# Kernel optimization log

Measured on AMD Instinct MI355X. Metric: run time of the kernel, lower is better.

## Reference

```python
import jax, jax.numpy as jnp
import numpy as np

B, S, D = 4, 4096, 1024

def setup_inputs() -> dict:
    key = jax.random.key(0)
    ks = jax.random.split(key, 5)
    scale = 1.0 / np.sqrt(D)
    return {
        "query": jax.random.normal(ks[0], (B, S, D), dtype=jnp.float32),
        "key": jax.random.normal(ks[1], (B, S, D), dtype=jnp.float32),
        "value": jax.random.normal(ks[2], (B, S, D), dtype=jnp.float32),
        "W": jax.random.normal(ks[3], (D, D), dtype=jnp.float32) * scale,  # torch Linear weight [out,in]
        "b": jax.random.normal(ks[4], (D,), dtype=jnp.float32) * 0.01,
    }

def reference(query, key, value, W, b):
    # shared projection (same_embd=True): q = Q W^T + b, same W,b for k,v
    q = jnp.einsum('bsd,od->bso', query, W) + b
    k = jnp.einsum('bsd,od->bso', key, W) + b
    v = jnp.einsum('bsd,od->bso', value, W) + b
    # unscaled dot-product attention (scaled=False default)
    a = jnp.einsum('bto,bso->bts', q, k)  # [B, tgt, src]
    attn = jax.nn.softmax(a, axis=2)
    output = jnp.einsum('bts,bso->bto', attn, v)
    return (output, attn)
```

## Files before the change

### kernel.cpp

```cpp
#include <hip/hip_runtime.h>
#include <hip/hip_bf16.h>
#include <hip/hip_fp16.h>

#define BD 4
#define SS 4096
#define DD 1024
#define RTOT (BD*SS)

typedef _Float16 f16;
typedef __attribute__((ext_vector_type(8))) _Float16 f16x8;
typedef __attribute__((ext_vector_type(4))) float f32x4;

static __device__ __forceinline__ unsigned short f2h(float f) {
  f16 h = (f16)f;
  return __builtin_bit_cast(unsigned short, h);
}
static __device__ __forceinline__ float h2f(unsigned short u) {
  return (float)__builtin_bit_cast(f16, u);
}

static __device__ __forceinline__ void gload16(const void* g, void* l) {
  __builtin_amdgcn_global_load_lds(
      (const __attribute__((address_space(1))) unsigned int*)g,
      (__attribute__((address_space(3))) unsigned int*)l, 16, 0, 0);
}

__global__ __launch_bounds__(256)
void convx_kernel(const float* __restrict__ q, const float* __restrict__ k,
                  const float* __restrict__ v,
                  unsigned short* __restrict__ xq, unsigned short* __restrict__ xk,
                  unsigned short* __restrict__ xv) {
  const float* src = blockIdx.z == 0 ? q : (blockIdx.z == 1 ? k : v);
  unsigned short* dst = blockIdx.z == 0 ? xq : (blockIdx.z == 1 ? xk : xv);
  const int n4 = RTOT * DD / 4;
  for (int i = blockIdx.x * 256 + threadIdx.x; i < n4; i += gridDim.x * 256) {
    float4 x = reinterpret_cast<const float4*>(src)[i];
    ushort4 h;
    h.x = f2h(x.x); h.y = f2h(x.y); h.z = f2h(x.z); h.w = f2h(x.w);
    reinterpret_cast<ushort4*>(dst)[i] = h;
  }
}

__global__ void split_w_kernel(const float* __restrict__ W,
                               unsigned short* __restrict__ Wh,
                               unsigned short* __restrict__ Wl) {
  int i = (blockIdx.x * 256 + threadIdx.x) * 4;
  float4 x = *reinterpret_cast<const float4*>(W + i);
  ushort4 h, l;
  h.x = f2h(x.x); l.x = f2h(x.x - h2f(h.x));
  h.y = f2h(x.y); l.y = f2h(x.y - h2f(h.y));
  h.z = f2h(x.z); l.z = f2h(x.z - h2f(h.z));
  h.w = f2h(x.w); l.w = f2h(x.w - h2f(h.w));
  *reinterpret_cast<ushort4*>(Wh + i) = h;
  *reinterpret_cast<ushort4*>(Wl + i) = l;
}

template<int TERMS, int EPI>
__global__ __launch_bounds__(512, 2)
void proj_one(const unsigned short* __restrict__ Xf,
              const unsigned short* __restrict__ Wh,
              const unsigned short* __restrict__ Wl,
              const float* __restrict__ bias,
              unsigned short* __restrict__ O1, unsigned short* __restrict__ O2)
{
  constexpr int OPS = 1 + TERMS;
  __shared__ unsigned short lds[2 * OPS][8192];
  const int tid = threadIdx.x, lane = tid & 63, wid = tid >> 6;
  const int t0 = blockIdx.x * 256;
  const int n0 = blockIdx.y * 256;

  const int sfr = (tid >> 2) & 15;
  const int scc = (tid & 3) ^ ((sfr >> 1) & 3);
  const int srowl = (tid >> 6) * 16 + sfr;
  const size_t aoff = (size_t)(t0 + srowl) * DD + scc * 8;
  const size_t boff = (size_t)(n0 + srowl) * DD + scc * 8;
  const int l0s = tid * 8;
  const int l1s = 4096 + tid * 8;

#define PSTAGE(cur, k0)  do { \
    gload16(Xf + aoff + (k0),          &lds[(cur)*OPS+0][l0s]); \
    gload16(Xf + aoff + 131072 + (k0), &lds[(cur)*OPS+0][l1s]); \
    gload16(Wh + boff + (k0),          &lds[(cur)*OPS+1][l0s]); \
    gload16(Wh + boff + 131072 + (k0), &lds[(cur)*OPS+1][l1s]); \
    if (TERMS == 2) { \
      gload16(Wl + boff + (k0),          &lds[(cur)*OPS+2][l0s]); \
      gload16(Wl + boff + 131072 + (k0), &lds[(cur)*OPS+2][l1s]); \
    } \
  } while (0)

  const int wr = wid >> 2, wc = wid & 3;
  const int rfr = lane & 15, rcc = lane >> 4;
  const int lp8 = (rfr * 4 + (rcc ^ ((rfr >> 1) & 3))) * 8;

  f32x4 acc[8][4] = {};

  int cur = 0;
  PSTAGE(0, 0);
  __syncthreads();

  for (int t = 0; t < 32; ++t) {
    if (t < 31) PSTAGE(cur ^ 1, (t + 1) * 32);

    f16x8 bhf[4], blf[4];
#pragma unroll
    for (int n = 0; n < 4; ++n) {
      bhf[n] = *reinterpret_cast<const f16x8*>(&lds[cur * OPS + 1][(wc * 4 + n) * 512 + lp8]);
      if (TERMS == 2)
        blf[n] = *reinterpret_cast<const f16x8*>(&lds[cur * OPS + 2][(wc * 4 + n) * 512 + lp8]);
    }
#pragma unroll
    for (int h = 0; h < 2; ++h) {
      f16x8 ahf[4];
#pragma unroll
      for (int m = 0; m < 4; ++m)
        ahf[m] = *reinterpret_cast<const f16x8*>(&lds[cur * OPS + 0][(wr * 8 + h * 4 + m) * 512 + lp8]);
      __builtin_amdgcn_s_setprio(1);
#pragma unroll
      for (int m = 0; m < 4; ++m)
#pragma unroll
        for (int n = 0; n < 4; ++n) {
          acc[h * 4 + m][n] = __builtin_amdgcn_mfma_f32_16x16x32_f16(ahf[m], bhf[n], acc[h * 4 + m][n], 0, 0, 0);
          if (TERMS == 2)
            acc[h * 4 + m][n] = __builtin_amdgcn_mfma_f32_16x16x32_f16(ahf[m], blf[n], acc[h * 4 + m][n], 0, 0, 0);
        }
      __builtin_amdgcn_s_setprio(0);
    }
    __syncthreads();
    cur ^= 1;
  }
#undef PSTAGE

  const int col = lane & 15, rb = (lane >> 4) * 4;
#pragma unroll
  for (int m = 0; m < 8; ++m)
#pragma unroll
    for (int n = 0; n < 4; ++n) {
      int oc = n0 + wc * 64 + n * 16 + col;
      float bv = bias[oc];
      if (EPI == 2) {
        int tr = t0 + wr * 128 + m * 16 + rb;
        int bb = tr >> 12, s = tr & (SS - 1);
        ushort4 h;
        h.x = f2h(acc[m][n][0] + bv);
        h.y = f2h(acc[m][n][1] + bv);
        h.z = f2h(acc[m][n][2] + bv);
        h.w = f2h(acc[m][n][3] + bv);
        *reinterpret_cast<ushort4*>(O1 + ((size_t)(bb * DD + oc)) * SS + s) = h;
      } else {
#pragma unroll
        for (int q = 0; q < 4; ++q) {
          int tr = t0 + wr * 128 + m * 16 + rb + q;
          float p = acc[m][n][q] + bv;
          if (EPI == 0) {
            O1[(size_t)tr * DD + oc] = f2h(p);
          } else {
            unsigned short h = f2h(p);
            O1[(size_t)tr * DD + oc] = h;
            O2[(size_t)tr * DD + oc] = f2h(p - h2f(h));
          }
        }
      }
    }
}

__global__ __launch_bounds__(512, 2)
void logits_v3(const unsigned short* __restrict__ qf,
               const unsigned short* __restrict__ kh, const unsigned short* __restrict__ kl,
               float* __restrict__ out)
{
  __shared__ unsigned short lds[6][8192];
  const int tid = threadIdx.x, lane = tid & 63, wid = tid >> 6;

  int bid = blockIdx.x;
  int swz = (bid & 7) * 128 + (bid >> 3);
  const int b = swz >> 8;
  const int r = swz & 255;
  const int t0 = (r >> 4) * 256, s0 = (r & 15) * 256;

  const unsigned short* qB  = qf + (size_t)b * SS * DD;
  const unsigned short* khB = kh + (size_t)b * SS * DD;
  const unsigned short* klB = kl + (size_t)b * SS * DD;

  const int sfr = (tid >> 2) & 15;
  const int scc = (tid & 3) ^ ((sfr >> 1) & 3);
  const int srowl = (tid >> 6) * 16 + sfr;
  const size_t qoff0 = (size_t)(t0 + srowl) * DD + scc * 8;
  const size_t koff0 = (size_t)(s0 + srowl) * DD + scc * 8;
  const int l0s = tid * 8;
  const int l1s = 4096 + tid * 8;

#define STAGE(cur, k0)  do { \
    gload16(qB  + qoff0 + (k0),          &lds[(cur)*3+0][l0s]); \
    gload16(qB  + qoff0 + 131072 + (k0), &lds[(cur)*3+0][l1s]); \
    gload16(khB + koff0 + (k0),          &lds[(cur)*3+1][l0s]); \
    gload16(khB + koff0 + 131072 + (k0), &lds[(cur)*3+1][l1s]); \
    gload16(klB + koff0 + (k0),          &lds[(cur)*3+2][l0s]); \
    gload16(klB + koff0 + 131072 + (k0), &lds[(cur)*3+2][l1s]); \
  } while (0)

  const int wr = wid >> 2, wc = wid & 3;
  const int rfr = lane & 15, rcc = lane >> 4;
  const int lp8 = (rfr * 4 + (rcc ^ ((rfr >> 1) & 3))) * 8;

  f32x4 acc[8][4] = {};

  int cur = 0;
  STAGE(0, 0);
  __syncthreads();

  for (int t = 0; t < 32; ++t) {
    if (t < 31) STAGE(cur ^ 1, (t + 1) * 32);

    f16x8 bhf[4], blf[4];
#pragma unroll
    for (int n = 0; n < 4; ++n) {
      bhf[n] = *reinterpret_cast<const f16x8*>(&lds[cur * 3 + 1][(wc * 4 + n) * 512 + lp8]);
      blf[n] = *reinterpret_cast<const f16x8*>(&lds[cur * 3 + 2][(wc * 4 + n) * 512 + lp8]);
    }
#pragma unroll
    for (int h = 0; h < 2; ++h) {
      f16x8 ahf[4];
#pragma unroll
      for (int m = 0; m < 4; ++m)
        ahf[m] = *reinterpret_cast<const f16x8*>(&lds[cur * 3 + 0][(wr * 8 + h * 4 + m) * 512 + lp8]);
      __builtin_amdgcn_s_setprio(1);
#pragma unroll
      for (int m = 0; m < 4; ++m)
#pragma unroll
        for (int n = 0; n < 4; ++n) {
          acc[h * 4 + m][n] = __builtin_amdgcn_mfma_f32_16x16x32_f16(ahf[m], bhf[n], acc[h * 4 + m][n], 0, 0, 0);
          acc[h * 4 + m][n] = __builtin_amdgcn_mfma_f32_16x16x32_f16(ahf[m], blf[n], acc[h * 4 + m][n], 0, 0, 0);
        }
      __builtin_amdgcn_s_setprio(0);
    }
    __syncthreads();
    cur ^= 1;
  }
#undef STAGE

  const int col = lane & 15, rb = (lane >> 4) * 4;
#pragma unroll
  for (int m = 0; m < 8; ++m)
#pragma unroll
    for (int n = 0; n < 4; ++n) {
      int s = s0 + wc * 64 + n * 16 + col;
#pragma unroll
      for (int q = 0; q < 4; ++q) {
        int tr = t0 + wr * 128 + m * 16 + rb + q;
        out[((size_t)b * SS + tr) * SS + s] = acc[m][n][q];
      }
    }
}

__global__ __launch_bounds__(256)
void softmax_kernel(float* __restrict__ attn) {
  float* rp = attn + (size_t)blockIdx.x * SS;
  const int tid = threadIdx.x, lane = tid & 63, wid = tid >> 6;
  float v[16];
  float m = -1e30f;
#pragma unroll
  for (int i = 0; i < 4; ++i) {
    float4 x = *reinterpret_cast<const float4*>(rp + i * 1024 + tid * 4);
    v[i * 4 + 0] = x.x; v[i * 4 + 1] = x.y; v[i * 4 + 2] = x.z; v[i * 4 + 3] = x.w;
    m = fmaxf(m, fmaxf(fmaxf(x.x, x.y), fmaxf(x.z, x.w)));
  }
#pragma unroll
  for (int off = 32; off; off >>= 1) m = fmaxf(m, __shfl_xor(m, off));
  __shared__ float redm[4], reds[4];
  if (lane == 0) redm[wid] = m;
  __syncthreads();
  m = fmaxf(fmaxf(redm[0], redm[1]), fmaxf(redm[2], redm[3]));
  float sum = 0.f;
#pragma unroll
  for (int i = 0; i < 16; ++i) { v[i] = __expf(v[i] - m); sum += v[i]; }
#pragma unroll
  for (int off = 32; off; off >>= 1) sum += __shfl_xor(sum, off);
  if (lane == 0) reds[wid] = sum;
  __syncthreads();
  float inv = 1.0f / (reds[0] + reds[1] + reds[2] + reds[3]);
#pragma unroll
  for (int i = 0; i < 4; ++i) {
    float4 x;
    x.x = v[i * 4 + 0] * inv; x.y = v[i * 4 + 1] * inv;
    x.z = v[i * 4 + 2] * inv; x.w = v[i * 4 + 3] * inv;
    *reinterpret_cast<float4*>(rp + i * 1024 + tid * 4) = x;
  }
}

__global__ __launch_bounds__(512)
void pv_v3(const float* __restrict__ attn, const unsigned short* __restrict__ vT,
           float* __restrict__ out)
{
  __shared__ unsigned short As[128][40];
  __shared__ unsigned short Bs[16384];
  const int tid = threadIdx.x, lane = tid & 63, wid = tid >> 6;

  int bx = blockIdx.x;
  bx = (bx & 7) * 4 + (bx >> 3);
  const int t0 = bx * 128;
  const int nH = blockIdx.y * 512;
  const int b = blockIdx.z;
  const float* aB = attn + ((size_t)b * SS + t0) * SS;
  const unsigned short* vB = vT + ((size_t)b * DD + nH) * SS;

  const int wr = wid >> 2, wc = wid & 3;

  const int sfr = (tid >> 2) & 15;
  const int scc = (tid & 3) ^ ((sfr >> 1) & 3);
  const int brow = (tid >> 6) * 16 + sfr;

  f32x4 acc[4][8] = {};

  for (int s0 = 0; s0 < SS; s0 += 32) {
    __syncthreads();
#pragma unroll
    for (int rnd = 0; rnd < 2; ++rnd) {
      int e = rnd * 512 + tid;
      int r = e >> 3, c = (e & 7) * 4;
      float4 x = *reinterpret_cast<const float4*>(aB + (size_t)r * SS + s0 + c);
      ushort4 h;
      h.x = f2h(x.x); h.y = f2h(x.y); h.z = f2h(x.z); h.w = f2h(x.w);
      *reinterpret_cast<ushort4*>(&As[r][c]) = h;
    }
#pragma unroll
    for (int g = 0; g < 4; ++g)
      gload16(vB + (size_t)(brow + g * 128) * SS + s0 + scc * 8,
              &Bs[0] + (size_t)g * 4096 + (size_t)tid * 8);
    __syncthreads();

    f16x8 a[4], bb[8];
    const int fr = lane & 15, kb = (lane >> 4) * 8;
    const int lp8 = (fr * 4 + ((lane >> 4) ^ ((fr >> 1) & 3))) * 8;
#pragma unroll
    for (int m = 0; m < 4; ++m)
      a[m] = *reinterpret_cast<const f16x8*>(&As[wr * 64 + m * 16 + fr][kb]);
#pragma unroll
    for (int n = 0; n < 8; ++n)
      bb[n] = *reinterpret_cast<const f16x8*>(&Bs[(wc * 8 + n) * 512 + lp8]);

    __builtin_amdgcn_s_setprio(1);
#pragma unroll
    for (int m = 0; m < 4; ++m)
#pragma unroll
      for (int n = 0; n < 8; ++n)
        acc[m][n] = __builtin_amdgcn_mfma_f32_16x16x32_f16(a[m], bb[n], acc[m][n], 0, 0, 0);
    __builtin_amdgcn_s_setprio(0);
  }

  const int col = lane & 15, rb = (lane >> 4) * 4;
#pragma unroll
  for (int m = 0; m < 4; ++m)
#pragma unroll
    for (int n = 0; n < 8; ++n) {
      int o = nH + wc * 128 + n * 16 + col;
#pragma unroll
      for (int q = 0; q < 4; ++q) {
        int t = t0 + wr * 64 + m * 16 + rb + q;
        out[((size_t)b * SS + t) * DD + o] = acc[m][n][q];
      }
    }
}

extern "C" void kernel_launch(void* const* d_in, const int* in_sizes, int n_in,
                              void* d_out, int out_size, void* d_ws, size_t ws_size,
                              hipStream_t stream) {
  const float* query = (const float*)d_in[0];
  const float* key   = (const float*)d_in[1];
  const float* value = (const float*)d_in[2];
  const float* W     = (const float*)d_in[3];
  const float* bias  = (const float*)d_in[4];

  float* out  = (float*)d_out;
  float* attn = out + (size_t)BD * SS * DD;

  unsigned short* Whf = (unsigned short*)d_ws;
  unsigned short* Wlf = Whf + (size_t)DD * DD;
  unsigned short* xq  = Wlf + (size_t)DD * DD;
  unsigned short* xk  = xq  + (size_t)RTOT * DD;
  unsigned short* xv  = xk  + (size_t)RTOT * DD;
  unsigned short* qfb = xv  + (size_t)RTOT * DD;
  unsigned short* khi = qfb + (size_t)RTOT * DD;
  unsigned short* klo = khi + (size_t)RTOT * DD;
  unsigned short* vT  = xq;

  convx_kernel<<<dim3(2048, 1, 3), 256, 0, stream>>>(query, key, value, xq, xk, xv);
  split_w_kernel<<<DD * DD / (256 * 4), 256, 0, stream>>>(W, Whf, Wlf);

  dim3 gp(RTOT / 256, DD / 256);
  proj_one<2, 0><<<gp, 512, 0, stream>>>(xq, Whf, Wlf, bias, qfb, nullptr);
  proj_one<2, 1><<<gp, 512, 0, stream>>>(xk, Whf, Wlf, bias, khi, klo);
  proj_one<1, 2><<<gp, 512, 0, stream>>>(xv, Whf, nullptr, bias, vT, nullptr);

  logits_v3<<<(SS / 256) * (SS / 256) * BD, 512, 0, stream>>>(qfb, khi, klo, attn);
  softmax_kernel<<<RTOT, 256, 0, stream>>>(attn);
  pv_v3<<<dim3(SS / 128, DD / 512, BD), 512, 0, stream>>>(attn, vT, out);
}
```

Baseline: 812.0 us.

## Double-buffer PV kernel and halve row tile to 64 for occupancy

The attention-times-V kernel now double-buffers its LDS tiles. The next V tile is loaded asynchronously and the next fp32 attention slice is prefetched into registers while MFMAs run on the current buffer, which drops one barrier per iteration. The row tile shrinks from 128 to 64, so each wave holds a 64x64 accumulator instead of 64x128. Launch bounds request two blocks per CU and the grid doubles in x. This aims to hide global-load latency and raise occupancy, at the cost of re-reading V twice as often across blocks.

```diff
diff --git a/kernel.cpp b/kernel.cpp
--- a/kernel.cpp
+++ b/kernel.cpp
@@ -287,75 +287,88 @@
   }
 }
 
-__global__ __launch_bounds__(512)
-void pv_v3(const float* __restrict__ attn, const unsigned short* __restrict__ vT,
+__global__ __launch_bounds__(512, 2)
+void pv_v4(const float* __restrict__ attn, const unsigned short* __restrict__ vT,
            float* __restrict__ out)
 {
-  __shared__ unsigned short As[128][40];
-  __shared__ unsigned short Bs[16384];
+  __shared__ unsigned short As[2][64][40];
+  __shared__ unsigned short Bs[2][16384];
   const int tid = threadIdx.x, lane = tid & 63, wid = tid >> 6;
 
-  int bx = blockIdx.x;
-  bx = (bx & 7) * 4 + (bx >> 3);
-  const int t0 = bx * 128;
+  int bid = blockIdx.x;
+  int bx = (bid & 7) * 8 + (bid >> 3);
+  const int t0 = bx * 64;
   const int nH = blockIdx.y * 512;
   const int b = blockIdx.z;
   const float* aB = attn + ((size_t)b * SS + t0) * SS;
   const unsigned short* vB = vT + ((size_t)b * DD + nH) * SS;
 
-  const int wr = wid >> 2, wc = wid & 3;
-
+  const int arow = tid >> 3, acol = (tid & 7) * 4;
   const int sfr = (tid >> 2) & 15;
   const int scc = (tid & 3) ^ ((sfr >> 1) & 3);
   const int brow = (tid >> 6) * 16 + sfr;
 
-  f32x4 acc[4][8] = {};
-
-  for (int s0 = 0; s0 < SS; s0 += 32) {
-    __syncthreads();
-#pragma unroll
-    for (int rnd = 0; rnd < 2; ++rnd) {
-      int e = rnd * 512 + tid;
-      int r = e >> 3, c = (e & 7) * 4;
-      float4 x = *reinterpret_cast<const float4*>(aB + (size_t)r * SS + s0 + c);
-      ushort4 h;
-      h.x = f2h(x.x); h.y = f2h(x.y); h.z = f2h(x.z); h.w = f2h(x.w);
-      *reinterpret_cast<ushort4*>(&As[r][c]) = h;
-    }
-#pragma unroll
-    for (int g = 0; g < 4; ++g)
-      gload16(vB + (size_t)(brow + g * 128) * SS + s0 + scc * 8,
-              &Bs[0] + (size_t)g * 4096 + (size_t)tid * 8);
-    __syncthreads();
-
-    f16x8 a[4], bb[8];
+  f32x4 acc[4][4] = {};
+  float4 areg;
+
+#define PVB_LOAD(buf, s0) do { \
+    _Pragma("unroll") \
+    for (int g = 0; g < 4; ++g) \
+      gload16(vB + (size_t)(brow + g * 128) * SS + (s0) + scc * 8, \
+              &Bs[buf][0] + (size_t)g * 4096 + (size_t)tid * 8); \
+  } while (0)
+#define PVA_WRITE(buf) do { \
+    ushort4 h; \
+    h.x = f2h(areg.x); h.y = f2h(areg.y); h.z = f2h(areg.z); h.w = f2h(areg.w); \
+    *reinterpret_cast<ushort4*>(&As[buf][arow][acol]) = h; \
+  } while (0)
+
+  PVB_LOAD(0, 0);
+  areg = *reinterpret_cast<const float4*>(aB + (size_t)arow * SS + acol);
+  PVA_WRITE(0);
+  __syncthreads();
+
+  int cur = 0;
+  for (int it = 0; it < 128; ++it) {
+    if (it < 127) {
+      PVB_LOAD(cur ^ 1, (it + 1) * 32);
+      areg = *reinterpret_cast<const float4*>(aB + (size_t)arow * SS + (it + 1) * 32 + acol);
+    }
+
+    f16x8 a[4], bb[4];
     const int fr = lane & 15, kb = (lane >> 4) * 8;
     const int lp8 = (fr * 4 + ((lane >> 4) ^ ((fr >> 1) & 3))) * 8;
 #pragma unroll
     for (int m = 0; m < 4; ++m)
-      a[m] = *reinterpret_cast<const f16x8*>(&As[wr * 64 + m * 16 + fr][kb]);
-#pragma unroll
-    for (int n = 0; n < 8; ++n)
-      bb[n] = *reinterpret_cast<const f16x8*>(&Bs[(wc * 8 + n) * 512 + lp8]);
+      a[m] = *reinterpret_cast<const f16x8*>(&As[cur][m * 16 + fr][kb]);
+#pragma unroll
+    for (int n = 0; n < 4; ++n)
+      bb[n] = *reinterpret_cast<const f16x8*>(&Bs[cur][(wid * 4 + n) * 512 + lp8]);
 
     __builtin_amdgcn_s_setprio(1);
 #pragma unroll
     for (int m = 0; m < 4; ++m)
 #pragma unroll
-      for (int n = 0; n < 8; ++n)
+      for (int n = 0; n < 4; ++n)
         acc[m][n] = __builtin_amdgcn_mfma_f32_16x16x32_f16(a[m], bb[n], acc[m][n], 0, 0, 0);
     __builtin_amdgcn_s_setprio(0);
-  }
+
+    if (it < 127) PVA_WRITE(cur ^ 1);
+    __syncthreads();
+    cur ^= 1;
+  }
+#undef PVB_LOAD
+#undef PVA_WRITE
 
   const int col = lane & 15, rb = (lane >> 4) * 4;
 #pragma unroll
   for (int m = 0; m < 4; ++m)
 #pragma unroll
-    for (int n = 0; n < 8; ++n) {
-      int o = nH + wc * 128 + n * 16 + col;
+    for (int n = 0; n < 4; ++n) {
+      int o = nH + wid * 64 + n * 16 + col;
 #pragma unroll
       for (int q = 0; q < 4; ++q) {
-        int t = t0 + wr * 64 + m * 16 + rb + q;
+        int t = t0 + m * 16 + rb + q;
         out[((size_t)b * SS + t) * DD + o] = acc[m][n][q];
       }
     }
@@ -393,5 +406,5 @@
 
   logits_v3<<<(SS / 256) * (SS / 256) * BD, 512, 0, stream>>>(qfb, khi, klo, attn);
   softmax_kernel<<<RTOT, 256, 0, stream>>>(attn);
-  pv_v3<<<dim3(SS / 128, DD / 512, BD), 512, 0, stream>>>(attn, vT, out);
-}
+  pv_v4<<<dim3(SS / 64, DD / 512, BD), 512, 0, stream>>>(attn, vT, out);
+}
```

Measured after the change: 811.4 us. No clear change (-0.1%).

## Double-buffer PV GEMM with register-prefetched attn and 256x256 tiles

Applied to the files above, without the earlier changes.

Rewrites the attention-times-V kernel to use 256x256 output tiles with a K step of 64, double-buffered LDS, and a register prefetch of the next fp32 attn tile. That tile is converted to fp16 and written to LDS after the MFMAs, which overlaps global loads with compute and halves the barriers per K. A new 1D block swizzle groups tiles across batch for cache locality. The cost is heavier register pressure (32 accumulators plus 8 float4 prefetch registers) and 128KB of LDS per block, which may limit occupancy.

```diff
diff --git a/kernel.cpp b/kernel.cpp
--- a/kernel.cpp
+++ b/kernel.cpp
@@ -288,74 +288,115 @@
 }
 
 __global__ __launch_bounds__(512)
-void pv_v3(const float* __restrict__ attn, const unsigned short* __restrict__ vT,
+void pv_v5(const float* __restrict__ attn, const unsigned short* __restrict__ vT,
            float* __restrict__ out)
 {
-  __shared__ unsigned short As[128][40];
-  __shared__ unsigned short Bs[16384];
+  __shared__ unsigned short lds[8][8192];
   const int tid = threadIdx.x, lane = tid & 63, wid = tid >> 6;
 
-  int bx = blockIdx.x;
-  bx = (bx & 7) * 4 + (bx >> 3);
-  const int t0 = bx * 128;
-  const int nH = blockIdx.y * 512;
-  const int b = blockIdx.z;
+  int bid = blockIdx.x;
+  int swz = (bid & 7) * 32 + (bid >> 3);
+  const int b = swz >> 6, rem = swz & 63;
+  const int t0 = (rem >> 2) * 256;
+  const int n0 = (rem & 3) * 256;
   const float* aB = attn + ((size_t)b * SS + t0) * SS;
-  const unsigned short* vB = vT + ((size_t)b * DD + nH) * SS;
-
-  const int wr = wid >> 2, wc = wid & 3;
+  const unsigned short* vB = vT + ((size_t)b * DD + n0) * SS;
 
   const int sfr = (tid >> 2) & 15;
   const int scc = (tid & 3) ^ ((sfr >> 1) & 3);
-  const int brow = (tid >> 6) * 16 + sfr;
-
-  f32x4 acc[4][8] = {};
-
-  for (int s0 = 0; s0 < SS; s0 += 32) {
+  const int srowl = (tid >> 6) * 16 + sfr;
+  const size_t row0 = (size_t)srowl * SS;
+  const size_t row1 = (size_t)(srowl + 128) * SS;
+  const int l0s = tid * 8, l1s = 4096 + tid * 8;
+
+  const int wr = wid >> 2, wc = wid & 3;
+  const int rfr = lane & 15, rcc = lane >> 4;
+  const int lp8 = (rfr * 4 + (rcc ^ ((rfr >> 1) & 3))) * 8;
+
+  f32x4 acc[8][4] = {};
+  float4 ar[8];
+
+#define PV5_BLOAD(buf, k0) do { \
+    gload16(vB + row0 + (k0) + scc * 8,      &lds[(buf)*4+2][l0s]); \
+    gload16(vB + row1 + (k0) + scc * 8,      &lds[(buf)*4+2][l1s]); \
+    gload16(vB + row0 + (k0) + 32 + scc * 8, &lds[(buf)*4+3][l0s]); \
+    gload16(vB + row1 + (k0) + 32 + scc * 8, &lds[(buf)*4+3][l1s]); \
+  } while (0)
+
+#define PV5_ALOAD(k0) do { \
+    ar[0] = *reinterpret_cast<const float4*>(aB + row0 + (k0) + scc * 8); \
+    ar[1] = *reinterpret_cast<const float4*>(aB + row0 + (k0) + scc * 8 + 4); \
+    ar[2] = *reinterpret_cast<const float4*>(aB + row1 + (k0) + scc * 8); \
+    ar[3] = *reinterpret_cast<const float4*>(aB + row1 + (k0) + scc * 8 + 4); \
+    ar[4] = *reinterpret_cast<const float4*>(aB + row0 + (k0) + 32 + scc * 8); \
+    ar[5] = *reinterpret_cast<const float4*>(aB + row0 + (k0) + 32 + scc * 8 + 4); \
+    ar[6] = *reinterpret_cast<const float4*>(aB + row1 + (k0) + 32 + scc * 8); \
+    ar[7] = *reinterpret_cast<const float4*>(aB + row1 + (k0) + 32 + scc * 8 + 4); \
+  } while (0)
+
+#define PV5_AWRITE(buf) do { \
+    _Pragma("unroll") \
+    for (int p = 0; p < 4; ++p) { \
+      int s = p >> 1, hh = p & 1; \
+      ushort4 u0, u1; \
+      u0.x = f2h(ar[p*2].x);   u0.y = f2h(ar[p*2].y); \
+      u0.z = f2h(ar[p*2].z);   u0.w = f2h(ar[p*2].w); \
+      u1.x = f2h(ar[p*2+1].x); u1.y = f2h(ar[p*2+1].y); \
+      u1.z = f2h(ar[p*2+1].z); u1.w = f2h(ar[p*2+1].w); \
+      unsigned short* d = &lds[(buf)*4 + s][(hh ? l1s : l0s)]; \
+      *reinterpret_cast<ushort4*>(d)     = u0; \
+      *reinterpret_cast<ushort4*>(d + 4) = u1; \
+    } \
+  } while (0)
+
+  int cur = 0;
+  PV5_BLOAD(0, 0);
+  PV5_ALOAD(0);
+  PV5_AWRITE(0);
+  __syncthreads();
+
+  for (int it = 0; it < 64; ++it) {
+    if (it < 63) { PV5_BLOAD(cur ^ 1, (it + 1) * 64); PV5_ALOAD((it + 1) * 64); }
+
+#pragma unroll
+    for (int s = 0; s < 2; ++s) {
+      f16x8 bf[4];
+#pragma unroll
+      for (int n = 0; n < 4; ++n)
+        bf[n] = *reinterpret_cast<const f16x8*>(&lds[cur * 4 + 2 + s][(wc * 4 + n) * 512 + lp8]);
+#pragma unroll
+      for (int h = 0; h < 2; ++h) {
+        f16x8 af[4];
+#pragma unroll
+        for (int m = 0; m < 4; ++m)
+          af[m] = *reinterpret_cast<const f16x8*>(&lds[cur * 4 + s][(wr * 8 + h * 4 + m) * 512 + lp8]);
+        __builtin_amdgcn_s_setprio(1);
+#pragma unroll
+        for (int m = 0; m < 4; ++m)
+#pragma unroll
+          for (int n = 0; n < 4; ++n)
+            acc[h * 4 + m][n] = __builtin_amdgcn_mfma_f32_16x16x32_f16(af[m], bf[n], acc[h * 4 + m][n], 0, 0, 0);
+        __builtin_amdgcn_s_setprio(0);
+      }
+    }
+
+    if (it < 63) PV5_AWRITE(cur ^ 1);
     __syncthreads();
-#pragma unroll
-    for (int rnd = 0; rnd < 2; ++rnd) {
-      int e = rnd * 512 + tid;
-      int r = e >> 3, c = (e & 7) * 4;
-      float4 x = *reinterpret_cast<const float4*>(aB + (size_t)r * SS + s0 + c);
-      ushort4 h;
-      h.x = f2h(x.x); h.y = f2h(x.y); h.z = f2h(x.z); h.w = f2h(x.w);
-      *reinterpret_cast<ushort4*>(&As[r][c]) = h;
-    }
-#pragma unroll
-    for (int g = 0; g < 4; ++g)
-      gload16(vB + (size_t)(brow + g * 128) * SS + s0 + scc * 8,
-              &Bs[0] + (size_t)g * 4096 + (size_t)tid * 8);
-    __syncthreads();
-
-    f16x8 a[4], bb[8];
-    const int fr = lane & 15, kb = (lane >> 4) * 8;
-    const int lp8 = (fr * 4 + ((lane >> 4) ^ ((fr >> 1) & 3))) * 8;
-#pragma unroll
-    for (int m = 0; m < 4; ++m)
-      a[m] = *reinterpret_cast<const f16x8*>(&As[wr * 64 + m * 16 + fr][kb]);
-#pragma unroll
-    for (int n = 0; n < 8; ++n)
-      bb[n] = *reinterpret_cast<const f16x8*>(&Bs[(wc * 8 + n) * 512 + lp8]);
-
-    __builtin_amdgcn_s_setprio(1);
-#pragma unroll
-    for (int m = 0; m < 4; ++m)
-#pragma unroll
-      for (int n = 0; n < 8; ++n)
-        acc[m][n] = __builtin_amdgcn_mfma_f32_16x16x32_f16(a[m], bb[n], acc[m][n], 0, 0, 0);
-    __builtin_amdgcn_s_setprio(0);
-  }
+    cur ^= 1;
+  }
+#undef PV5_BLOAD
+#undef PV5_ALOAD
+#undef PV5_AWRITE
 
   const int col = lane & 15, rb = (lane >> 4) * 4;
 #pragma unroll
-  for (int m = 0; m < 4; ++m)
-#pragma unroll
-    for (int n = 0; n < 8; ++n) {
-      int o = nH + wc * 128 + n * 16 + col;
+  for (int m = 0; m < 8; ++m)
+#pragma unroll
+    for (int n = 0; n < 4; ++n) {
+      int o = n0 + wc * 64 + n * 16 + col;
 #pragma unroll
       for (int q = 0; q < 4; ++q) {
-        int t = t0 + wr * 64 + m * 16 + rb + q;
+        int t = t0 + wr * 128 + m * 16 + rb + q;
         out[((size_t)b * SS + t) * DD + o] = acc[m][n][q];
       }
     }
@@ -393,5 +434,5 @@
 
   logits_v3<<<(SS / 256) * (SS / 256) * BD, 512, 0, stream>>>(qfb, khi, klo, attn);
   softmax_kernel<<<RTOT, 256, 0, stream>>>(attn);
-  pv_v3<<<dim3(SS / 128, DD / 512, BD), 512, 0, stream>>>(attn, vT, out);
-}
+  pv_v5<<<(SS / 256) * (DD / 256) * BD, 512, 0, stream>>>(attn, vT, out);
+}
```

After: 734.4 us. -9.6%, faster.
